# Optimization experiments

Measured on AMD Instinct MI355X. Metric: run time of the kernel, lower is better.

Reference implementation:

```python
import jax, jax.numpy as jnp
import numpy as np

KS = (7, 7)
ST = (3, 3)
PD = (3, 3)
DIM = 512
HID = 1960  # 40 * 49, divisible by kernel_shape


def _patch_flat_idx(out_h, out_w):
    kh, kw = KS; sh, sw = ST; ph, pw = PD
    oh = (out_h + 2 * ph - kh) // sh + 1
    ow = (out_w + 2 * pw - kw) // sw + 1
    Wp = out_w + 2 * pw
    iy = jnp.arange(kh)[:, None, None, None] + (jnp.arange(oh) * sh)[None, None, :, None]
    ix = jnp.arange(kw)[None, :, None, None] + (jnp.arange(ow) * sw)[None, None, None, :]
    # (kh, kw, oh, ow) flat index into padded image
    return (iy * Wp + ix), oh, ow


def fold(patches, out_h, out_w):
    # patches: (B, C*kh*kw, L) -> (B, C, out_h, out_w), overlap-add like F.fold
    kh, kw = KS; ph, pw = PD
    idx, oh, ow = _patch_flat_idx(out_h, out_w)
    B, CK, L = patches.shape
    C = CK // (kh * kw)
    Hp, Wp = out_h + 2 * ph, out_w + 2 * pw
    p = patches.reshape(B, C, kh, kw, oh, ow)
    out = jnp.zeros((B, C, Hp * Wp), patches.dtype)
    out = out.at[:, :, idx.reshape(-1)].add(p.reshape(B, C, -1))
    return out.reshape(B, C, Hp, Wp)[:, :, ph:ph + out_h, pw:pw + out_w]


def unfold(img, out_h, out_w):
    # img: (B, C, H, W) -> (B, C*kh*kw, L), like F.unfold
    kh, kw = KS; ph, pw = PD
    idx, oh, ow = _patch_flat_idx(out_h, out_w)
    B, C = img.shape[:2]
    imgp = jnp.pad(img, ((0, 0), (0, 0), (ph, ph), (pw, pw)))
    flat = imgp.reshape(B, C, -1)
    g = flat[:, :, idx.reshape(-1)].reshape(B, C, kh, kw, oh, ow)
    return g.reshape(B, C * kh * kw, oh * ow)


def setup_inputs() -> dict:
    key = jax.random.key(0)
    k1, k2, k3, k4, k5 = jax.random.split(key, 5)
    x = jax.random.normal(k1, (2, 5760, DIM), dtype=jnp.float32)
    W1 = jax.random.normal(k2, (HID, DIM), dtype=jnp.float32) * 0.02
    b1 = jax.random.normal(k3, (HID,), dtype=jnp.float32) * 0.02
    W2 = jax.random.normal(k4, (DIM, HID), dtype=jnp.float32) * 0.02
    b2 = jax.random.normal(k5, (DIM,), dtype=jnp.float32) * 0.02
    return {"x": x, "W1": W1, "b1": b1, "W2": W2, "b2": b2, "out_h": 60, "out_w": 108}


def reference(x, W1, b1, W2, b2, out_h, out_w):
    kh, kw = KS; sh, sw = ST; ph, pw = PD
    oh = (out_h + 2 * ph - kh) // sh + 1
    ow = (out_w + 2 * pw - kw) // sw + 1
    n_vecs = oh * ow
    h = jnp.einsum('bnd,hd->bnh', x, W1) + b1          # (b, n, HID)
    b_, n, c = h.shape
    p = h.reshape(-1, n_vecs, c).transpose(0, 2, 1)     # (B', c, L)
    folded = fold(p, out_h, out_w)                      # (B', c//49, H, W)
    ones = jnp.ones((p.shape[0], kh * kw, n_vecs), h.dtype)
    norm = fold(ones, out_h, out_w)                     # (B', 1, H, W)
    y = unfold(folded / norm, out_h, out_w)             # (B', c, L)
    y = y.transpose(0, 2, 1).reshape(b_, n, c)
    out = jnp.einsum('bnh,dh->bnd', jax.nn.gelu(y, approximate=False), W2) + b2
    return out
```

## Files before the change

kernel.cpp:

```cpp
#include <hip/hip_runtime.h>
#include <cmath>

#define M_ROWS   11520
#define DIM      512
#define HID      1960
#define HIDP     2048
#define KP2      1984
#define OH       20
#define OW       36
#define LVEC     720
#define NCH      40
#define BPRIME   16
#define HP       66
#define WP       114

typedef unsigned short u16;
typedef __bf16 bf16x8 __attribute__((ext_vector_type(8)));
typedef float  f32x4  __attribute__((ext_vector_type(4)));

__device__ __forceinline__ u16 f2bf(float f) {
    unsigned u = __float_as_uint(f);
    u += 0x7fffu + ((u >> 16) & 1u);
    return (u16)(u >> 16);
}
__device__ __forceinline__ float bf2f(u16 h) {
    return __uint_as_float(((unsigned)h) << 16);
}

__device__ __forceinline__ void gload_lds16(const void* g, void* l) {
    __builtin_amdgcn_global_load_lds(
        (const __attribute__((address_space(1))) void*)g,
        (__attribute__((address_space(3))) void*)l, 16, 0, 0);
}

__global__ __launch_bounds__(256) void cvt_x(const float* __restrict__ src,
                                             u16* __restrict__ dst, int n) {
    int i = (blockIdx.x * 256 + threadIdx.x) * 4;
    if (i < n) {
        float4 v = *(const float4*)(src + i);
        ushort4 o;
        o.x = f2bf(v.x); o.y = f2bf(v.y); o.z = f2bf(v.z); o.w = f2bf(v.w);
        *(ushort4*)(dst + i) = o;
    }
}

__global__ __launch_bounds__(256) void cvt_w1(const float* __restrict__ src,
                                              u16* __restrict__ dst) {
    int i = (blockIdx.x * 256 + threadIdx.x) * 4;
    ushort4 o;
    if (i < HID * DIM) {
        float4 v = *(const float4*)(src + i);
        o.x = f2bf(v.x); o.y = f2bf(v.y); o.z = f2bf(v.z); o.w = f2bf(v.w);
    } else {
        o.x = o.y = o.z = o.w = 0;
    }
    *(ushort4*)(dst + i) = o;
}

__global__ __launch_bounds__(256) void cvt_w2(const float* __restrict__ src,
                                              u16* __restrict__ dst) {
    int i = (blockIdx.x * 256 + threadIdx.x) * 4;
    int d = i / HIDP, c = i % HIDP;
    ushort4 o;
    if (c < HID) {
        float4 v = *(const float4*)(src + d * HID + c);
        o.x = f2bf(v.x); o.y = f2bf(v.y); o.z = f2bf(v.z); o.w = f2bf(v.w);
    } else {
        o.x = o.y = o.z = o.w = 0;
    }
    *(ushort4*)(dst + i) = o;
}

template <int OUT_BF16, int BN>
__global__ __launch_bounds__(256) void gemm_bt(const u16* __restrict__ A,
                                               const u16* __restrict__ B,
                                               const float* __restrict__ bias,
                                               int biasN, void* __restrict__ Cout,
                                               int N, int K, int ldk) {
    constexpr int WN = BN / 2;
    constexpr int NU = WN / 16;

    __shared__ u16 sA[128 * 64];
    __shared__ u16 sB[BN * 64];

    const int tid  = threadIdx.x;
    const int ntn  = N / BN;
    const int NB   = gridDim.x;
    const int v    = (blockIdx.x & 7) * (NB >> 3) + (blockIdx.x >> 3);
    const int bm   = v / ntn;
    const int bn   = v - bm * ntn;
    const int lane = tid & 63;
    const int wv   = tid >> 6;
    const int wm   = (wv >> 1) * 64;
    const int wn   = (wv & 1) * WN;
    const int r    = lane & 15;
    const int quad = lane >> 4;

    const size_t Arow0 = (size_t)bm * 128 * ldk;
    const size_t Brow0 = (size_t)bn * BN * ldk;

    f32x4 acc[4][NU] = {};

    for (int kt = 0; kt < K; kt += 64) {
        __syncthreads();
#pragma unroll
        for (int i = 0; i < 4; i++) {
            int e   = i * 256 + tid;
            int row = e >> 3;
            int cp  = e & 7;
            int cg  = cp ^ (row & 7);
            gload_lds16(A + Arow0 + (size_t)row * ldk + kt + cg * 8, (char*)sA + e * 16);
        }
#pragma unroll
        for (int i = 0; i < (BN * 8) / 256; i++) {
            int e   = i * 256 + tid;
            int row = e >> 3;
            int cp  = e & 7;
            int cg  = cp ^ (row & 7);
            gload_lds16(B + Brow0 + (size_t)row * ldk + kt + cg * 8, (char*)sB + e * 16);
        }
        __syncthreads();
#pragma unroll
        for (int kk = 0; kk < 2; kk++) {
            bf16x8 af[4], bg[NU];
#pragma unroll
            for (int t = 0; t < 4; t++) {
                int row = wm + t * 16 + r;
                int c   = (kk * 4 + quad) ^ (row & 7);
                af[t] = *(const bf16x8*)(sA + row * 64 + c * 8);
            }
#pragma unroll
            for (int u = 0; u < NU; u++) {
                int row = wn + u * 16 + r;
                int c   = (kk * 4 + quad) ^ (row & 7);
                bg[u] = *(const bf16x8*)(sB + row * 64 + c * 8);
            }
#pragma unroll
            for (int t = 0; t < 4; t++)
#pragma unroll
                for (int u = 0; u < NU; u++)
                    acc[t][u] = __builtin_amdgcn_mfma_f32_16x16x32_bf16(
                        af[t], bg[u], acc[t][u], 0, 0, 0);
        }
    }

    const int gm0 = bm * 128 + wm;
    const int gn0 = bn * BN + wn;
#pragma unroll
    for (int u = 0; u < NU; u++) {
        int gn = gn0 + u * 16 + r;
        float bv = (gn < biasN) ? bias[gn] : 0.0f;
#pragma unroll
        for (int t = 0; t < 4; t++) {
            int gm = gm0 + t * 16 + quad * 4;
#pragma unroll
            for (int q = 0; q < 4; q++) {
                float v2 = acc[t][u][q] + bv;
                if (OUT_BF16)
                    ((u16*)Cout)[(size_t)(gm + q) * N + gn] = f2bf(v2);
                else
                    ((float*)Cout)[(size_t)(gm + q) * N + gn] = v2;
            }
        }
    }
}

__global__ __launch_bounds__(256) void midA_fold(const u16* __restrict__ hg,
                                                 u16* __restrict__ G) {
    __shared__ u16 sh[12 * OW * 49];

    const int b  = blockIdx.x;
    const int bp = b / (NCH * 2);
    const int rr = b - bp * (NCH * 2);
    const int ch = rr >> 1;
    const int s  = rr & 1;
    const int o0 = s * 10;
    const int lo = s * 8;
    const int n0 = bp * LVEC;
    const int c0 = ch * 49;
    const int tid = threadIdx.x;

    for (int i = tid; i < 12 * OW * 49; i += 256) {
        int l = i / 49, k = i - l * 49;
        sh[i] = hg[(size_t)(n0 + lo * OW + l) * HIDP + c0 + k];
    }
    __syncthreads();

    u16* Gb = G + (size_t)(bp * NCH + ch) * (HP * WP) + 3 * o0 * WP;
    for (int p = tid; p < 34 * WP; p += 256) {
        int pyr = p / WP;
        int px  = p - pyr * WP;
        int py  = pyr + 3 * o0;
        float val = 0.0f;
        if (py >= 3 && py <= 62 && px >= 3 && px <= 110) {
            int ky0 = py % 3, kx0 = px % 3;
            int cy = 0, cx = 0;
            float sum = 0.0f;
#pragma unroll
            for (int dy = 0; dy < 3; dy++) {
                int ky = ky0 + 3 * dy, ry = py - ky;
                if (ky <= 6 && ry >= 0 && ry <= 57) cy++;
            }
#pragma unroll
            for (int dx = 0; dx < 3; dx++) {
                int kx = kx0 + 3 * dx, rx = px - kx;
                if (kx <= 6 && rx >= 0 && rx <= 105) cx++;
            }
#pragma unroll
            for (int dy = 0; dy < 3; dy++) {
                int ky = ky0 + 3 * dy, ry = py - ky;
                bool vy = (ky <= 6 && ry >= 0 && ry <= 57);
                int lrow = ry / 3 - lo;
#pragma unroll
                for (int dx = 0; dx < 3; dx++) {
                    int kx = kx0 + 3 * dx, rx = px - kx;
                    if (vy && kx <= 6 && rx >= 0 && rx <= 105) {
                        int ox = rx / 3;
                        sum += bf2f(sh[(lrow * OW + ox) * 49 + ky * 7 + kx]);
                    }
                }
            }
            float m = sum / (float)(cy * cx);
            val = 0.5f * m * (1.0f + erff(m * 0.70710678118654752f));
        }
        Gb[p] = f2bf(val);
    }
}

__global__ __launch_bounds__(256) void midB_unfold(const u16* __restrict__ G,
                                                   u16* __restrict__ hg) {
    __shared__ u16 sG[34 * WP];

    const int b  = blockIdx.x;
    const int bp = b / (NCH * 2);
    const int rr = b - bp * (NCH * 2);
    const int ch = rr >> 1;
    const int s  = rr & 1;
    const int o0 = s * 10;
    const int n0 = bp * LVEC + o0 * OW;
    const int c0 = ch * 49;
    const int tid = threadIdx.x;

    const u16* Gb = G + (size_t)(bp * NCH + ch) * (HP * WP) + 3 * o0 * WP;
    for (int p = tid; p < 34 * WP; p += 256) sG[p] = Gb[p];
    __syncthreads();

    for (int i = tid; i < 10 * OW * 49; i += 256) {
        int l = i / 49, k = i - l * 49;
        int ky = k / 7, kx = k - ky * 7;
        int oy = l / OW, ox = l - oy * OW;
        hg[(size_t)(n0 + l) * HIDP + c0 + k] = sG[(3 * oy + ky) * WP + kx + 3 * ox];
    }
}

extern "C" void kernel_launch(void* const* d_in, const int* in_sizes, int n_in,
                              void* d_out, int out_size, void* d_ws, size_t ws_size,
                              hipStream_t stream) {
    (void)in_sizes; (void)n_in; (void)out_size; (void)ws_size;
    const float* x  = (const float*)d_in[0];
    const float* W1 = (const float*)d_in[1];
    const float* b1 = (const float*)d_in[2];
    const float* W2 = (const float*)d_in[3];
    const float* b2 = (const float*)d_in[4];
    float* out = (float*)d_out;

    char* ws = (char*)d_ws;
    u16* xb  = (u16*)(ws);
    u16* W1b = (u16*)(ws + 11796480);
    u16* W2b = (u16*)(ws + 11796480 + 2097152);
    u16* hg  = (u16*)(ws + 11796480 + 2097152 + 2097152);
    u16* G   = xb;

    cvt_x <<<(M_ROWS * DIM) / (256 * 4), 256, 0, stream>>>(x, xb, M_ROWS * DIM);
    cvt_w1<<<(HIDP * DIM) / (256 * 4), 256, 0, stream>>>(W1, W1b);
    cvt_w2<<<(DIM * HIDP) / (256 * 4), 256, 0, stream>>>(W2, W2b);

    gemm_bt<1, 128><<<(M_ROWS / 128) * (HIDP / 128), 256, 0, stream>>>(
        xb, W1b, b1, HID, (void*)hg, HIDP, DIM, DIM);

    midA_fold<<<BPRIME * NCH * 2, 256, 0, stream>>>(hg, G);
    midB_unfold<<<BPRIME * NCH * 2, 256, 0, stream>>>(G, hg);

    gemm_bt<0, 64><<<(M_ROWS / 128) * (DIM / 64), 256, 0, stream>>>(
        hg, W2b, b2, DIM, (void*)out, DIM, KP2, HIDP);
}
```

Measured before the change: 224.6 us.

## Split fold kernel into four row slabs with per-column precomputed offsets

```diff
diff --git a/kernel.cpp b/kernel.cpp
--- a/kernel.cpp
+++ b/kernel.cpp
@@ -167,63 +167,73 @@
 
 __global__ __launch_bounds__(256) void midA_fold(const u16* __restrict__ hg,
                                                  u16* __restrict__ G) {
-    __shared__ u16 sh[12 * OW * 49];
+    __shared__ u16 sh[7 * OW * 49];
 
     const int b  = blockIdx.x;
-    const int bp = b / (NCH * 2);
-    const int rr = b - bp * (NCH * 2);
-    const int ch = rr >> 1;
-    const int s  = rr & 1;
-    const int o0 = s * 10;
-    const int lo = s * 8;
+    const int bp = b / (NCH * 4);
+    const int rr = b - bp * (NCH * 4);
+    const int ch = rr >> 2;
+    const int s  = rr & 3;
+    const int lo    = (s == 0) ? 0 : (5 * s - 2);
+    const int nload = (s == 0) ? 5 : 7;
+    const int row0  = 15 * s;
+    const int nrows = (s == 3) ? 21 : 15;
     const int n0 = bp * LVEC;
     const int c0 = ch * 49;
     const int tid = threadIdx.x;
 
-    for (int i = tid; i < 12 * OW * 49; i += 256) {
+    for (int i = tid; i < nload * OW * 49; i += 256) {
         int l = i / 49, k = i - l * 49;
         sh[i] = hg[(size_t)(n0 + lo * OW + l) * HIDP + c0 + k];
     }
     __syncthreads();
 
-    u16* Gb = G + (size_t)(bp * NCH + ch) * (HP * WP) + 3 * o0 * WP;
-    for (int p = tid; p < 34 * WP; p += 256) {
-        int pyr = p / WP;
-        int px  = p - pyr * WP;
-        int py  = pyr + 3 * o0;
+    const int px = tid & 127;
+    const int rg = tid >> 7;
+    if (px >= WP) return;
+
+    const bool pxin = (px >= 3) && (px <= 110);
+    const int kx0 = px % 3;
+    int  ct[3];
+    bool vx[3];
+    int  cx = 0;
+#pragma unroll
+    for (int dx = 0; dx < 3; dx++) {
+        int kx = kx0 + 3 * dx, rx = px - kx;
+        bool ok = pxin && (kx <= 6) && (rx >= 0) && (rx <= 105);
+        vx[dx] = ok;
+        ct[dx] = ok ? ((rx / 3) * 49 + kx) : 0;
+        cx += ok ? 1 : 0;
+    }
+    const float fcx = (cx == 3) ? (1.0f / 3.0f) : ((cx == 2) ? 0.5f : 1.0f);
+
+    u16* Gb = G + (size_t)(bp * NCH + ch) * (HP * WP);
+    for (int ri = rg; ri < nrows; ri += 2) {
+        int py = row0 + ri;
         float val = 0.0f;
-        if (py >= 3 && py <= 62 && px >= 3 && px <= 110) {
-            int ky0 = py % 3, kx0 = px % 3;
-            int cy = 0, cx = 0;
+        if (pxin && py >= 3 && py <= 62) {
+            int ky0 = py % 3;
             float sum = 0.0f;
+            int cy = 0;
 #pragma unroll
             for (int dy = 0; dy < 3; dy++) {
                 int ky = ky0 + 3 * dy, ry = py - ky;
-                if (ky <= 6 && ry >= 0 && ry <= 57) cy++;
-            }
-#pragma unroll
-            for (int dx = 0; dx < 3; dx++) {
-                int kx = kx0 + 3 * dx, rx = px - kx;
-                if (kx <= 6 && rx >= 0 && rx <= 105) cx++;
-            }
-#pragma unroll
-            for (int dy = 0; dy < 3; dy++) {
-                int ky = ky0 + 3 * dy, ry = py - ky;
-                bool vy = (ky <= 6 && ry >= 0 && ry <= 57);
-                int lrow = ry / 3 - lo;
-#pragma unroll
-                for (int dx = 0; dx < 3; dx++) {
-                    int kx = kx0 + 3 * dx, rx = px - kx;
-                    if (vy && kx <= 6 && rx >= 0 && rx <= 105) {
-                        int ox = rx / 3;
-                        sum += bf2f(sh[(lrow * OW + ox) * 49 + ky * 7 + kx]);
-                    }
+                if (ky <= 6 && ry >= 0 && ry <= 57) {
+                    int rt = (ry / 3 - lo) * (OW * 49) + ky * 7;
+                    cy++;
+                    float v0 = bf2f(sh[rt + ct[0]]);
+                    float v1 = bf2f(sh[rt + ct[1]]);
+                    float v2 = bf2f(sh[rt + ct[2]]);
+                    sum += vx[0] ? v0 : 0.0f;
+                    sum += vx[1] ? v1 : 0.0f;
+                    sum += vx[2] ? v2 : 0.0f;
                 }
             }
-            float m = sum / (float)(cy * cx);
+            float fcy = (cy == 3) ? (1.0f / 3.0f) : ((cy == 2) ? 0.5f : 1.0f);
+            float m = sum * fcx * fcy;
             val = 0.5f * m * (1.0f + erff(m * 0.70710678118654752f));
         }
-        Gb[p] = f2bf(val);
+        Gb[py * WP + px] = f2bf(val);
     }
 }
 
@@ -278,7 +288,7 @@
     gemm_bt<1, 128><<<(M_ROWS / 128) * (HIDP / 128), 256, 0, stream>>>(
         xb, W1b, b1, HID, (void*)hg, HIDP, DIM, DIM);
 
-    midA_fold<<<BPRIME * NCH * 2, 256, 0, stream>>>(hg, G);
+    midA_fold<<<BPRIME * NCH * 4, 256, 0, stream>>>(hg, G);
     midB_unfold<<<BPRIME * NCH * 2, 256, 0, stream>>>(G, hg);
 
     gemm_bt<0, 64><<<(M_ROWS / 128) * (DIM / 64), 256, 0, stream>>>(
```

Result: faster. 209.5 us (-6.8%).
